# Kernel tuning notes

Hardware: AMD Instinct MI355X
Metric: run time of the kernel (lower is better)

The kernel has to match this reference:

```python
import jax, jax.numpy as jnp
import numpy as np

STRIDE = (1, 2, 2)
PADDING = ((2, 2), (3, 3), (3, 3))


def setup_inputs() -> dict:
    key = jax.random.key(0)
    kx, kw, kb = jax.random.split(key, 3)
    x = jax.random.normal(kx, (8, 3, 16, 112, 112), dtype=jnp.float32)
    weight = jax.random.normal(kw, (64, 3, 5, 7, 7), dtype=jnp.float32)
    bias = jax.random.normal(kb, (64,), dtype=jnp.float32)
    return {"x": x, "weight": weight, "bias": bias}


def reference(x, weight, bias):
    # NCDHW input, OIDHW weight -> NCDHW output; same math as the
    # torch module's explicit slice-multiply-sum conv3d.
    out = jax.lax.conv_general_dilated(
        x, weight,
        window_strides=STRIDE,
        padding=PADDING,
        dimension_numbers=("NCDHW", "OIDHW", "NCDHW"),
    )
    out = out + bias[None, :, None, None, None]
    return out
```

## Files before the change

### kernel.cpp

```cpp
#include <hip/hip_runtime.h>


typedef __attribute__((ext_vector_type(8)))  short short8;
typedef __attribute__((ext_vector_type(4)))  float f32x4;
typedef __attribute__((ext_vector_type(16))) float f32x16;

#define CI 3
#define DI 16
#define HI 112
#define WI 112
#define CO 64
#define DO_ 16
#define HO 56
#define WO 56
#define HW_IN 12544
#define DHWO 50176

#define NROW 105
#define NCH 27

#define XP_ROW 120
#define XP_H   119
#define XP_D   20
#define XPAD_BYTES  (8*3*XP_D*XP_H*XP_ROW*2)
#define WBUF_OFF    XPAD_BYTES
#define WS_NEED     (WBUF_OFF + NCH*4*64*16 + 4096)

#define SEG_SH 1080
#define SEG_DW 540
#define ROW_DW 60

__device__ __forceinline__ unsigned short f2bf(float f) {
    unsigned u = __float_as_uint(f);
    return (unsigned short)((u + 0x7FFFu + ((u >> 16) & 1u)) >> 16);
}
__device__ __forceinline__ unsigned pk_bf16(float a, float b) {
    unsigned r;
    asm("v_cvt_pk_bf16_f32 %0, %1, %2" : "=v"(r) : "v"(a), "v"(b));
    return r;
}

__device__ __forceinline__ constexpr int rb2(int r) {
    const int rc = (r > 104) ? 104 : r;
    const int c  = rc / 35;
    const int kd = (rc / 7) % 5;
    const int kh = rc % 7;
    return (c * 6 + kd) * SEG_DW + kh * ROW_DW;
}

#define XP_THREADS (8*3*XP_D*XP_H*15)
#define XP_BLOCKS  3347

__global__ void prep_all(const float* __restrict__ x, const float* __restrict__ wgt,
                         unsigned* __restrict__ xp, short8* __restrict__ wbuf) {
    if (blockIdx.x < XP_BLOCKS) {
        const int g = blockIdx.x * 256 + threadIdx.x;
        if (g >= XP_THREADS) return;
        const int s8 = g % 15;
        int r = g / 15;
        const int hp = r % XP_H; r /= XP_H;
        const int dp = r % XP_D; r /= XP_D;
        const int c  = r % 3;
        const int n  = r / 3;
        const int din = dp - 2, hin = hp - 3;
        const bool rowok = ((unsigned)din < (unsigned)DI) && ((unsigned)hin < (unsigned)HI);
        float v[8];
        const int w0 = 8 * s8 - 3;
        if (rowok && s8 >= 1 && s8 <= 13) {
            const float* xr = x + ((n * CI + c) * DI + din) * HW_IN + hin * WI + w0;
            #pragma unroll
            for (int j = 0; j < 8; ++j) v[j] = xr[j];
        } else if (rowok && (s8 == 0 || s8 == 14)) {
            const float* xr = x + ((n * CI + c) * DI + din) * HW_IN + hin * WI;
            #pragma unroll
            for (int j = 0; j < 8; ++j) {
                const int w = w0 + j;
                v[j] = ((unsigned)w < (unsigned)WI) ? xr[w] : 0.0f;
            }
        } else {
            #pragma unroll
            for (int j = 0; j < 8; ++j) v[j] = 0.0f;
        }
        uint4 o;
        o.x = pk_bf16(v[0], v[1]); o.y = pk_bf16(v[2], v[3]);
        o.z = pk_bf16(v[4], v[5]); o.w = pk_bf16(v[6], v[7]);
        *reinterpret_cast<uint4*>(xp + 4 * (size_t)g) = o;
    } else {
        const int t = (blockIdx.x - XP_BLOCKS) * 256 + threadIdx.x;
        const int lane = t & 63;
        const int cf   = t >> 6;
        const int q    = cf & 3;
        const int a    = q & 1;
        const int ks   = q >> 1;
        const int ch   = cf >> 2;
        const int l31  = lane & 31;
        const int hl   = lane >> 5;
        const int co   = a * 32 + l31;
        const int r    = ch * 4 + ks * 2 + hl;
        const int rc   = (r > 104) ? 104 : r;
        const int c    = rc / 35;
        const int kd   = (rc / 7) % 5;
        const int kh   = rc % 7;
        const float* wsrc = wgt + (((co * CI + c) * 5 + kd) * 7 + kh) * 7;
        short8 v;
        #pragma unroll
        for (int j = 0; j < 8; ++j) {
            float w = (r < NROW && j < 7) ? wsrc[j] : 0.0f;
            v[j] = (short)f2bf(w);
        }
        wbuf[(size_t)cf * 64 + lane] = v;
    }
}

#define MFMA32(A, B, C) __builtin_amdgcn_mfma_f32_32x32x16_bf16(A, B, C, 0, 0, 0)

__launch_bounds__(256, 4)
__global__ void conv3d_v13(const unsigned short* __restrict__ xpad,
                           const short8* __restrict__ wbuf,
                           const float* __restrict__ bias,
                           float* __restrict__ out) {
    __shared__ __align__(16) unsigned short xl[18 * SEG_SH + 128];

    const int tid = threadIdx.x;
    int b = ((blockIdx.x & 7) * 224) + (blockIdx.x >> 3);
    const int ht  = b % 28;  b /= 28;
    const int ddp = b & 7;
    const int n   = b >> 3;
    const int ho0 = ht * 2;
    const int dd0 = ddp * 2;

    const int lane = tid & 63;
    const int wid  = tid >> 6;

    {
        const size_t nb = (size_t)(n * CI) * XP_D;
        for (int s = wid; s < 18; s += 4) {
            const int c = s / 6;
            const int p = s - c * 6;
            const char* gsrc = (const char*)(xpad +
                ((nb + (size_t)c * XP_D + (dd0 + p)) * XP_H + 2 * ho0) * XP_ROW)
                + lane * 16;
            char* ldst = (char*)&xl[s * SEG_SH];
            __builtin_amdgcn_global_load_lds(
                (const __attribute__((address_space(1))) void*)(gsrc),
                (__attribute__((address_space(3))) void*)(ldst), 16, 0, 0);
            __builtin_amdgcn_global_load_lds(
                (const __attribute__((address_space(1))) void*)(gsrc + 1024),
                (__attribute__((address_space(3))) void*)(ldst + 1024), 16, 0, 0);
            if (lane < 7)
                __builtin_amdgcn_global_load_lds(
                    (const __attribute__((address_space(1))) void*)(gsrc + 2048),
                    (__attribute__((address_space(3))) void*)(ldst + 2048), 16, 0, 0);
        }
    }

    const int ddl = wid & 1;
    const int hoL = wid >> 1;
    const int l31 = lane & 31;
    const int hl  = lane >> 5;
    const int tspB = ddl * SEG_DW + hoL * (2 * ROW_DW) + l31;

    f32x16 acc[2][2];
    #pragma unroll
    for (int a = 0; a < 2; ++a) {
        f32x16 bv;
        #pragma unroll
        for (int g = 0; g < 16; ++g)
            bv[g] = bias[a * 32 + (g & 3) + 8 * (g >> 2) + 4 * hl];
        acc[a][0] = bv; acc[a][1] = bv;
    }

    const short8* wbp = wbuf + lane;
    const unsigned* xlu = reinterpret_cast<const unsigned*>(xl);

    union BxU { unsigned u[4]; short8 s; };
    short8 As[2][4];
    BxU    Bs[4];

    auto loadA = [&](int ch, int slot) {
        const int nq = (ch == NCH - 1) ? 2 : 4;
        #pragma unroll
        for (int q = 0; q < 4; ++q)
            if (q < nq) As[slot][q] = wbp[(ch * 4 + q) * 64];
    };
    auto loadB = [&](int ch) {
        const int nks = (ch == NCH - 1) ? 1 : 2;
        #pragma unroll
        for (int ks = 0; ks < 2; ++ks) {
            if (ks < nks) {
                const int r0 = ch * 4 + ks * 2;
                const int b0 = rb2(r0);
                const int b1 = rb2(r0 + 1);
                const int base = b0 + hl * (b1 - b0);
                const unsigned* xp = xlu + base + tspB;
                #pragma unroll
                for (int f = 0; f < 2; ++f) {
                    const unsigned* p = xp + f * 32;
                    Bs[ks * 2 + f].u[0] = p[0];
                    Bs[ks * 2 + f].u[1] = p[1];
                    Bs[ks * 2 + f].u[2] = p[2];
                    Bs[ks * 2 + f].u[3] = p[3];
                }
            }
        }
    };

    loadA(0, 0);
    __syncthreads();

    #pragma unroll
    for (int ch = 0; ch < NCH; ++ch) {
        loadB(ch);
        if (ch + 1 < NCH) loadA(ch + 1, (ch + 1) & 1);
        __builtin_amdgcn_s_setprio(1);
        const int s = ch & 1;
        #pragma unroll
        for (int a = 0; a < 2; ++a) {
            #pragma unroll
            for (int f = 0; f < 2; ++f) {
                acc[a][f] = MFMA32(As[s][0 + a], Bs[0 + f].s, acc[a][f]);
                if (ch != NCH - 1)
                    acc[a][f] = MFMA32(As[s][2 + a], Bs[2 + f].s, acc[a][f]);
            }
        }
        __builtin_amdgcn_s_setprio(0);
    }

    const int dd = dd0 + ddl;
    const int ho = ho0 + hoL;
    const size_t obase = (size_t)n * CO * DHWO + (size_t)dd * 3136 + ho * WO;
    #pragma unroll
    for (int f = 0; f < 2; ++f) {
        const int wo = f * 32 + l31;
        if (f == 0 || l31 < 24) {
            #pragma unroll
            for (int a = 0; a < 2; ++a) {
                #pragma unroll
                for (int g = 0; g < 16; ++g) {
                    const int co = a * 32 + (g & 3) + 8 * (g >> 2) + 4 * hl;
                    out[obase + (size_t)co * DHWO + wo] = acc[a][f][g];
                }
            }
        }
    }
}

#define FB_LR 13
#define FB_LROWS 234
#define FB_LWS 144
#define FB_XLSZ (FB_LROWS*FB_LWS)
#define MFMA16(A, B, C) __builtin_amdgcn_mfma_f32_16x16x32_bf16(A, B, C, 0, 0, 0)

__global__ void prep_weights_fb(const float* __restrict__ wgt, short8* __restrict__ wbuf) {
    const int t    = blockIdx.x * 64 + threadIdx.x;
    const int lane = t & 63;
    const int cf   = t >> 6;
    const int l15  = lane & 15;
    const int kgrp = lane >> 4;
    const int co   = (cf & 3) * 16 + l15;
    const int rr   = (cf >> 2) * 4 + kgrp;
    const int rc   = (rr < NROW) ? rr : (NROW - 1);
    const int c    = rc / 35;
    const int kd   = (rc / 7) % 5;
    const int kh   = rc % 7;
    const float* wsrc = wgt + (((co * CI + c) * 5 + kd) * 7 + kh) * 7;
    short8 v;
    #pragma unroll
    for (int j = 0; j < 8; ++j) {
        float w = (rr < NROW && j < 7) ? wsrc[j] : 0.0f;
        v[j] = (short)f2bf(w);
    }
    wbuf[(size_t)cf * 64 + lane] = v;
}

__launch_bounds__(512, 2)
__global__ void conv3d_mfma4(const float* __restrict__ x,
                             const short8* __restrict__ wbuf,
                             const float* __restrict__ bias,
                             float* __restrict__ out) {
    __shared__ unsigned short xl[FB_XLSZ];
    __shared__ int rowg[FB_LROWS];
    __shared__ unsigned short tabr[108];

    const int tid = threadIdx.x;
    int b = blockIdx.x;
    const int ht  = b % 14;  b /= 14;
    const int ddp = b % 8;
    const int n   = b / 8;
    const int ho0 = ht * 4;
    const int dd0 = ddp * 2;

    if (tid < FB_LROWS) {
        const int c   = tid / (6 * FB_LR);
        const int rem = tid - c * (6 * FB_LR);
        const int p   = rem / FB_LR;
        const int rl  = rem - p * FB_LR;
        const int din = dd0 - 2 + p;
        const int hin = 2 * ho0 - 3 + rl;
        const bool ok = ((unsigned)din < (unsigned)DI) && ((unsigned)hin < (unsigned)HI);
        rowg[tid] = ok ? ((n * CI + c) * DI + din) * HW_IN + hin * WI : -1;
    }
    if (tid < 108) {
        const int rc = (tid < NROW) ? tid : (NROW - 1);
        const int c  = rc / 35;
        const int kd = (rc / 7) % 5;
        const int kh = rc % 7;
        tabr[tid] = (unsigned short)(((c * 6 + kd) * FB_LR + kh) * FB_LWS);
    }
    __syncthreads();

    const int lane = tid & 63;
    const int wid  = tid >> 6;

    for (int row = wid; row < FB_LROWS; row += 8) {
        const int base = rowg[row];
        unsigned short* dst = &xl[row * FB_LWS];
        if (lane < 57) {
            float v0 = 0.0f, v1 = 0.0f;
            const int w0 = 2 * lane - 1;
            if (base >= 0) {
                if (lane >= 1)  v0 = x[base + w0];
                if (lane <= 55) v1 = x[base + w0 + 1];
            }
            *reinterpret_cast<unsigned*>(&dst[2 * lane + 2]) = pk_bf16(v0, v1);
        } else {
            const int dw = (lane == 57) ? 0 : lane;
            *reinterpret_cast<unsigned*>(&dst[2 * dw]) = 0u;
        }
    }
    __syncthreads();

    const int ddl  = wid & 1;
    const int hoL  = wid >> 1;
    const int l15  = lane & 15;
    const int kgrp = lane >> 4;
    const int woff = ddl * (FB_LR * FB_LWS) + hoL * (2 * FB_LWS);

    f32x4 acc[4][4];
    #pragma unroll
    for (int a = 0; a < 4; ++a) {
        f32x4 bv;
        #pragma unroll
        for (int r = 0; r < 4; ++r) bv[r] = bias[a * 16 + kgrp * 4 + r];
        #pragma unroll
        for (int f = 0; f < 4; ++f) acc[a][f] = bv;
    }

    const short8* wbp = wbuf + lane;
    short8 Acur[4], Anxt[4];
    #pragma unroll
    for (int a = 0; a < 4; ++a) Acur[a] = wbp[a * 64];
    int tb = (int)tabr[kgrp] + woff;

    const unsigned* xlu = reinterpret_cast<const unsigned*>(xl);

    for (int ch = 0; ch < NCH; ++ch) {
        int tbn = 0;
        if (ch + 1 < NCH) {
            tbn = (int)tabr[(ch + 1) * 4 + kgrp] + woff;
            #pragma unroll
            for (int a = 0; a < 4; ++a) Anxt[a] = wbp[((ch + 1) * 4 + a) * 64];
        }
        const unsigned* xp = xlu + (tb >> 1) + l15;
        union { unsigned u[4]; short8 s; } bx[4];
        #pragma unroll
        for (int f = 0; f < 4; ++f) {
            const unsigned* p = xp + f * 16;
            bx[f].u[0] = p[0]; bx[f].u[1] = p[1];
            bx[f].u[2] = p[2]; bx[f].u[3] = p[3];
        }
        #pragma unroll
        for (int f = 0; f < 4; ++f) {
            acc[0][f] = MFMA16(Acur[0], bx[f].s, acc[0][f]);
            acc[1][f] = MFMA16(Acur[1], bx[f].s, acc[1][f]);
            acc[2][f] = MFMA16(Acur[2], bx[f].s, acc[2][f]);
            acc[3][f] = MFMA16(Acur[3], bx[f].s, acc[3][f]);
        }
        tb = tbn;
        #pragma unroll
        for (int a = 0; a < 4; ++a) Acur[a] = Anxt[a];
    }

    const int dd = dd0 + ddl;
    const int ho = ho0 + hoL;
    #pragma unroll
    for (int f = 0; f < 4; ++f) {
        const int wo = f * 16 + l15;
        if (f < 3 || l15 < 8) {
            float* op = out + (((size_t)(n * CO) * DO_ + dd) * HO + ho) * WO + wo;
            #pragma unroll
            for (int a = 0; a < 4; ++a) {
                const int co = a * 16 + kgrp * 4;
                #pragma unroll
                for (int r = 0; r < 4; ++r)
                    op[(size_t)(co + r) * DHWO] = acc[a][f][r];
            }
        }
    }
}

extern "C" void kernel_launch(void* const* d_in, const int* in_sizes, int n_in,
                              void* d_out, int out_size, void* d_ws, size_t ws_size,
                              hipStream_t stream) {
    const float* x    = (const float*)d_in[0];
    const float* wgt  = (const float*)d_in[1];
    const float* bias = (const float*)d_in[2];
    float* out        = (float*)d_out;

    if (ws_size >= (size_t)WS_NEED) {
        unsigned* xpad = (unsigned*)d_ws;
        short8* wbuf   = (short8*)((char*)d_ws + WBUF_OFF);
        hipLaunchKernelGGL(prep_all, dim3(XP_BLOCKS + 27, 1, 1), dim3(256, 1, 1), 0,
                           stream, x, wgt, xpad, wbuf);
        hipLaunchKernelGGL(conv3d_v13, dim3(1792, 1, 1), dim3(256, 1, 1), 0, stream,
                           (const unsigned short*)xpad, wbuf, bias, out);
    } else {
        short8* wbuf = (short8*)d_ws;
        hipLaunchKernelGGL(prep_weights_fb, dim3(NCH * 4, 1, 1), dim3(64, 1, 1), 0,
                           stream, wgt, wbuf);
        hipLaunchKernelGGL(conv3d_mfma4, dim3(896, 1, 1), dim3(512, 1, 1), 0, stream,
                           x, wbuf, bias, out);
    }
}
```

Measured before the change: 67.69 us.

## Load conv input tiles directly from global memory, dropping LDS staging

The conv kernel no longer stages the padded input slab into shared memory with global_load_lds and a barrier. Each lane now reads its B fragments straight from the padded bf16 buffer in global memory as 16-byte vector loads. A three-slot register ring prefetches B two chunks ahead to hide the global latency. This removes the LDS fill and the __syncthreads, but it relies on L1/L2 for the heavy input reuse across overlapping windows and raises register pressure, so the launch bounds drop from 4 to 3 blocks per CU.

```diff
diff --git a/kernel.cpp b/kernel.cpp
--- a/kernel.cpp
+++ b/kernel.cpp
@@ -26,9 +26,10 @@
 #define WBUF_OFF    XPAD_BYTES
 #define WS_NEED     (WBUF_OFF + NCH*4*64*16 + 4096)
 
-#define SEG_SH 1080
-#define SEG_DW 540
 #define ROW_DW 60
+#define DP_DW  (XP_H*ROW_DW)
+#define C_DW   (XP_D*DP_DW)
+#define N_DW   (CI*C_DW)
 
 __device__ __forceinline__ unsigned short f2bf(float f) {
     unsigned u = __float_as_uint(f);
@@ -40,12 +41,12 @@
     return r;
 }
 
-__device__ __forceinline__ constexpr int rb2(int r) {
+__device__ __forceinline__ constexpr int G(int r) {
     const int rc = (r > 104) ? 104 : r;
     const int c  = rc / 35;
     const int kd = (rc / 7) % 5;
     const int kh = rc % 7;
-    return (c * 6 + kd) * SEG_DW + kh * ROW_DW;
+    return c * C_DW + kd * DP_DW + kh * ROW_DW;
 }
 
 #define XP_THREADS (8*3*XP_D*XP_H*15)
@@ -114,13 +115,11 @@
 
 #define MFMA32(A, B, C) __builtin_amdgcn_mfma_f32_32x32x16_bf16(A, B, C, 0, 0, 0)
 
-__launch_bounds__(256, 4)
-__global__ void conv3d_v13(const unsigned short* __restrict__ xpad,
+__launch_bounds__(256, 3)
+__global__ void conv3d_v16(const unsigned* __restrict__ xdw,
                            const short8* __restrict__ wbuf,
                            const float* __restrict__ bias,
                            float* __restrict__ out) {
-    __shared__ __align__(16) unsigned short xl[18 * SEG_SH + 128];
-
     const int tid = threadIdx.x;
     int b = ((blockIdx.x & 7) * 224) + (blockIdx.x >> 3);
     const int ht  = b % 28;  b /= 28;
@@ -132,33 +131,13 @@
     const int lane = tid & 63;
     const int wid  = tid >> 6;
 
-    {
-        const size_t nb = (size_t)(n * CI) * XP_D;
-        for (int s = wid; s < 18; s += 4) {
-            const int c = s / 6;
-            const int p = s - c * 6;
-            const char* gsrc = (const char*)(xpad +
-                ((nb + (size_t)c * XP_D + (dd0 + p)) * XP_H + 2 * ho0) * XP_ROW)
-                + lane * 16;
-            char* ldst = (char*)&xl[s * SEG_SH];
-            __builtin_amdgcn_global_load_lds(
-                (const __attribute__((address_space(1))) void*)(gsrc),
-                (__attribute__((address_space(3))) void*)(ldst), 16, 0, 0);
-            __builtin_amdgcn_global_load_lds(
-                (const __attribute__((address_space(1))) void*)(gsrc + 1024),
-                (__attribute__((address_space(3))) void*)(ldst + 1024), 16, 0, 0);
-            if (lane < 7)
-                __builtin_amdgcn_global_load_lds(
-                    (const __attribute__((address_space(1))) void*)(gsrc + 2048),
-                    (__attribute__((address_space(3))) void*)(ldst + 2048), 16, 0, 0);
-        }
-    }
-
     const int ddl = wid & 1;
     const int hoL = wid >> 1;
     const int l31 = lane & 31;
     const int hl  = lane >> 5;
-    const int tspB = ddl * SEG_DW + hoL * (2 * ROW_DW) + l31;
+    const int dd  = dd0 + ddl;
+    const int ho  = ho0 + hoL;
+    const int wbase = n * N_DW + dd * DP_DW + ho * (2 * ROW_DW) + l31;
 
     f32x16 acc[2][2];
     #pragma unroll
@@ -171,11 +150,11 @@
     }
 
     const short8* wbp = wbuf + lane;
-    const unsigned* xlu = reinterpret_cast<const unsigned*>(xl);
+    const unsigned* xw = xdw + wbase;
 
     union BxU { unsigned u[4]; short8 s; };
     short8 As[2][4];
-    BxU    Bs[4];
+    BxU    Bs[3][4];
 
     auto loadA = [&](int ch, int slot) {
         const int nq = (ch == NCH - 1) ? 2 : 4;
@@ -183,51 +162,50 @@
         for (int q = 0; q < 4; ++q)
             if (q < nq) As[slot][q] = wbp[(ch * 4 + q) * 64];
     };
-    auto loadB = [&](int ch) {
+    auto loadB = [&](int ch, int slot) {
         const int nks = (ch == NCH - 1) ? 1 : 2;
         #pragma unroll
         for (int ks = 0; ks < 2; ++ks) {
             if (ks < nks) {
                 const int r0 = ch * 4 + ks * 2;
-                const int b0 = rb2(r0);
-                const int b1 = rb2(r0 + 1);
-                const int base = b0 + hl * (b1 - b0);
-                const unsigned* xp = xlu + base + tspB;
+                const int g0 = G(r0);
+                const int g1 = G(r0 + 1);
+                const unsigned* p0 = xw + (g0 + hl * (g1 - g0));
                 #pragma unroll
                 for (int f = 0; f < 2; ++f) {
-                    const unsigned* p = xp + f * 32;
-                    Bs[ks * 2 + f].u[0] = p[0];
-                    Bs[ks * 2 + f].u[1] = p[1];
-                    Bs[ks * 2 + f].u[2] = p[2];
-                    Bs[ks * 2 + f].u[3] = p[3];
+                    uint4 v = *reinterpret_cast<const uint4*>(p0 + f * 32);
+                    Bs[slot][ks * 2 + f].u[0] = v.x;
+                    Bs[slot][ks * 2 + f].u[1] = v.y;
+                    Bs[slot][ks * 2 + f].u[2] = v.z;
+                    Bs[slot][ks * 2 + f].u[3] = v.w;
                 }
             }
         }
     };
 
     loadA(0, 0);
-    __syncthreads();
+    loadB(0, 0);
+    loadB(1, 1);
 
     #pragma unroll
     for (int ch = 0; ch < NCH; ++ch) {
-        loadB(ch);
+        if (ch + 2 < NCH) loadB(ch + 2, (ch + 2) % 3);
         if (ch + 1 < NCH) loadA(ch + 1, (ch + 1) & 1);
         __builtin_amdgcn_s_setprio(1);
-        const int s = ch & 1;
+        const int sA = ch & 1;
+        const int sB = ch % 3;
         #pragma unroll
         for (int a = 0; a < 2; ++a) {
             #pragma unroll
             for (int f = 0; f < 2; ++f) {
-                acc[a][f] = MFMA32(As[s][0 + a], Bs[0 + f].s, acc[a][f]);
+                acc[a][f] = MFMA32(As[sA][0 + a], Bs[sB][0 + f].s, acc[a][f]);
                 if (ch != NCH - 1)
-                    acc[a][f] = MFMA32(As[s][2 + a], Bs[2 + f].s, acc[a][f]);
+                    acc[a][f] = MFMA32(As[sA][2 + a], Bs[sB][2 + f].s, acc[a][f]);
             }
         }
         __builtin_amdgcn_s_setprio(0);
     }
 
-    const int dd = dd0 + ddl;
-    const int ho = ho0 + hoL;
     const size_t obase = (size_t)n * CO * DHWO + (size_t)dd * 3136 + ho * WO;
     #pragma unroll
     for (int f = 0; f < 2; ++f) {
@@ -412,8 +390,8 @@
         short8* wbuf   = (short8*)((char*)d_ws + WBUF_OFF);
         hipLaunchKernelGGL(prep_all, dim3(XP_BLOCKS + 27, 1, 1), dim3(256, 1, 1), 0,
                            stream, x, wgt, xpad, wbuf);
-        hipLaunchKernelGGL(conv3d_v13, dim3(1792, 1, 1), dim3(256, 1, 1), 0, stream,
-                           (const unsigned short*)xpad, wbuf, bias, out);
+        hipLaunchKernelGGL(conv3d_v16, dim3(1792, 1, 1), dim3(256, 1, 1), 0, stream,
+                           xpad, wbuf, bias, out);
     } else {
         short8* wbuf = (short8*)d_ws;
         hipLaunchKernelGGL(prep_weights_fb, dim3(NCH * 4, 1, 1), dim3(64, 1, 1), 0,
```

Measured after the change: 77.92 us. 1.15x slower.

## Double block to 512 threads, 4 output rows, stage weights in LDS

Applied to the files above, without the earlier changes.

Each block now covers four output rows instead of two using 8 waves, so the staged input halo (13 rows vs 9) is shared over more output rows. This cuts redundant global-to-LDS input traffic. Weight fragments move from per-wave global loads to a double-buffered LDS stage filled by global_load_lds, one wave per chunk. That adds a __syncthreads per chunk, which may stall the MFMA pipeline and lower overlap.

```diff
diff --git a/kernel.cpp b/kernel.cpp
--- a/kernel.cpp
+++ b/kernel.cpp
@@ -26,9 +26,11 @@
 #define WBUF_OFF    XPAD_BYTES
 #define WS_NEED     (WBUF_OFF + NCH*4*64*16 + 4096)
 
-#define SEG_SH 1080
-#define SEG_DW 540
-#define ROW_DW 60
+#define LR 13
+#define SEG_SH (LR*XP_ROW)
+#define SEG_DW (SEG_SH/2)
+#define ROW_DW (XP_ROW/2)
+#define ALDS_SH (18*SEG_SH + 128)
 
 __device__ __forceinline__ unsigned short f2bf(float f) {
     unsigned u = __float_as_uint(f);
@@ -113,20 +115,23 @@
 }
 
 #define MFMA32(A, B, C) __builtin_amdgcn_mfma_f32_32x32x16_bf16(A, B, C, 0, 0, 0)
-
-__launch_bounds__(256, 4)
-__global__ void conv3d_v13(const unsigned short* __restrict__ xpad,
+#define GLDS(src, dst) __builtin_amdgcn_global_load_lds( \
+    (const __attribute__((address_space(1))) void*)(src), \
+    (__attribute__((address_space(3))) void*)(dst), 16, 0, 0)
+
+__launch_bounds__(512, 4)
+__global__ void conv3d_v17(const unsigned short* __restrict__ xpad,
                            const short8* __restrict__ wbuf,
                            const float* __restrict__ bias,
                            float* __restrict__ out) {
-    __shared__ __align__(16) unsigned short xl[18 * SEG_SH + 128];
+    __shared__ __align__(16) unsigned short xl[ALDS_SH + 4096];
 
     const int tid = threadIdx.x;
-    int b = ((blockIdx.x & 7) * 224) + (blockIdx.x >> 3);
-    const int ht  = b % 28;  b /= 28;
+    int b = ((blockIdx.x & 7) * 112) + (blockIdx.x >> 3);
+    const int ht  = b % 14;  b /= 14;
     const int ddp = b & 7;
     const int n   = b >> 3;
-    const int ho0 = ht * 2;
+    const int ho0 = ht * 4;
     const int dd0 = ddp * 2;
 
     const int lane = tid & 63;
@@ -134,31 +139,32 @@
 
     {
         const size_t nb = (size_t)(n * CI) * XP_D;
-        for (int s = wid; s < 18; s += 4) {
+        for (int s = wid; s < 18; s += 8) {
             const int c = s / 6;
             const int p = s - c * 6;
             const char* gsrc = (const char*)(xpad +
                 ((nb + (size_t)c * XP_D + (dd0 + p)) * XP_H + 2 * ho0) * XP_ROW)
                 + lane * 16;
             char* ldst = (char*)&xl[s * SEG_SH];
-            __builtin_amdgcn_global_load_lds(
-                (const __attribute__((address_space(1))) void*)(gsrc),
-                (__attribute__((address_space(3))) void*)(ldst), 16, 0, 0);
-            __builtin_amdgcn_global_load_lds(
-                (const __attribute__((address_space(1))) void*)(gsrc + 1024),
-                (__attribute__((address_space(3))) void*)(ldst + 1024), 16, 0, 0);
-            if (lane < 7)
-                __builtin_amdgcn_global_load_lds(
-                    (const __attribute__((address_space(1))) void*)(gsrc + 2048),
-                    (__attribute__((address_space(3))) void*)(ldst + 2048), 16, 0, 0);
-        }
-    }
+            GLDS(gsrc, ldst);
+            GLDS(gsrc + 1024, ldst + 1024);
+            GLDS(gsrc + 2048, ldst + 2048);
+            if (lane < 3) GLDS(gsrc + 3072, ldst + 3072);
+        }
+    }
+    if (wid == 0) {
+        const char* gs = (const char*)wbuf + lane * 16;
+        char* ad = (char*)&xl[ALDS_SH];
+        GLDS(gs, ad); GLDS(gs + 1024, ad + 1024);
+        GLDS(gs + 2048, ad + 2048); GLDS(gs + 3072, ad + 3072);
+    }
+    __syncthreads();
 
     const int ddl = wid & 1;
-    const int hoL = wid >> 1;
+    const int hp  = wid >> 1;
     const int l31 = lane & 31;
     const int hl  = lane >> 5;
-    const int tspB = ddl * SEG_DW + hoL * (2 * ROW_DW) + l31;
+    const int tspB = ddl * SEG_DW + hp * (2 * ROW_DW) + l31;
 
     f32x16 acc[2][2];
     #pragma unroll
@@ -170,64 +176,57 @@
         acc[a][0] = bv; acc[a][1] = bv;
     }
 
-    const short8* wbp = wbuf + lane;
     const unsigned* xlu = reinterpret_cast<const unsigned*>(xl);
-
     union BxU { unsigned u[4]; short8 s; };
-    short8 As[2][4];
-    BxU    Bs[4];
-
-    auto loadA = [&](int ch, int slot) {
-        const int nq = (ch == NCH - 1) ? 2 : 4;
-        #pragma unroll
-        for (int q = 0; q < 4; ++q)
-            if (q < nq) As[slot][q] = wbp[(ch * 4 + q) * 64];
-    };
-    auto loadB = [&](int ch) {
-        const int nks = (ch == NCH - 1) ? 1 : 2;
+
+    #pragma unroll
+    for (int ch = 0; ch < NCH; ++ch) {
+        if (ch + 1 < NCH && wid == ((ch + 1) & 7)) {
+            const char* gs = (const char*)(wbuf + (size_t)(ch + 1) * 4 * 64) + lane * 16;
+            char* ad = (char*)&xl[ALDS_SH] + ((ch + 1) & 1) * 4096;
+            GLDS(gs, ad); GLDS(gs + 1024, ad + 1024);
+            GLDS(gs + 2048, ad + 2048); GLDS(gs + 3072, ad + 3072);
+        }
+        short8 As[4];
+        {
+            const char* ab = (const char*)&xl[ALDS_SH] + (ch & 1) * 4096 + lane * 16;
+            As[0] = *reinterpret_cast<const short8*>(ab);
+            As[1] = *reinterpret_cast<const short8*>(ab + 1024);
+            As[2] = *reinterpret_cast<const short8*>(ab + 2048);
+            As[3] = *reinterpret_cast<const short8*>(ab + 3072);
+        }
+        BxU Bs[4];
         #pragma unroll
         for (int ks = 0; ks < 2; ++ks) {
-            if (ks < nks) {
-                const int r0 = ch * 4 + ks * 2;
-                const int b0 = rb2(r0);
-                const int b1 = rb2(r0 + 1);
-                const int base = b0 + hl * (b1 - b0);
-                const unsigned* xp = xlu + base + tspB;
-                #pragma unroll
-                for (int f = 0; f < 2; ++f) {
-                    const unsigned* p = xp + f * 32;
-                    Bs[ks * 2 + f].u[0] = p[0];
-                    Bs[ks * 2 + f].u[1] = p[1];
-                    Bs[ks * 2 + f].u[2] = p[2];
-                    Bs[ks * 2 + f].u[3] = p[3];
-                }
-            }
-        }
-    };
-
-    loadA(0, 0);
-    __syncthreads();
-
-    #pragma unroll
-    for (int ch = 0; ch < NCH; ++ch) {
-        loadB(ch);
-        if (ch + 1 < NCH) loadA(ch + 1, (ch + 1) & 1);
+            const int r0 = ch * 4 + ks * 2;
+            const int b0 = rb2(r0);
+            const int b1 = rb2(r0 + 1);
+            const int base = b0 + hl * (b1 - b0);
+            const unsigned* xp = xlu + base + tspB;
+            #pragma unroll
+            for (int f = 0; f < 2; ++f) {
+                const unsigned* p = xp + f * 32;
+                Bs[ks * 2 + f].u[0] = p[0];
+                Bs[ks * 2 + f].u[1] = p[1];
+                Bs[ks * 2 + f].u[2] = p[2];
+                Bs[ks * 2 + f].u[3] = p[3];
+            }
+        }
         __builtin_amdgcn_s_setprio(1);
-        const int s = ch & 1;
         #pragma unroll
         for (int a = 0; a < 2; ++a) {
             #pragma unroll
             for (int f = 0; f < 2; ++f) {
-                acc[a][f] = MFMA32(As[s][0 + a], Bs[0 + f].s, acc[a][f]);
-                if (ch != NCH - 1)
-                    acc[a][f] = MFMA32(As[s][2 + a], Bs[2 + f].s, acc[a][f]);
+                acc[a][f] = MFMA32(As[0 + a], Bs[0 + f].s, acc[a][f]);
+                acc[a][f] = MFMA32(As[2 + a], Bs[2 + f].s, acc[a][f]);
             }
         }
         __builtin_amdgcn_s_setprio(0);
+        if (ch != NCH - 1) __syncthreads();
     }
 
     const int dd = dd0 + ddl;
-    const int ho = ho0 + hoL;
+    const int ho = ho0 + hp;
     const size_t obase = (size_t)n * CO * DHWO + (size_t)dd * 3136 + ho * WO;
     #pragma unroll
     for (int f = 0; f < 2; ++f) {
@@ -412,7 +411,7 @@
         short8* wbuf   = (short8*)((char*)d_ws + WBUF_OFF);
         hipLaunchKernelGGL(prep_all, dim3(XP_BLOCKS + 27, 1, 1), dim3(256, 1, 1), 0,
                            stream, x, wgt, xpad, wbuf);
-        hipLaunchKernelGGL(conv3d_v13, dim3(1792, 1, 1), dim3(256, 1, 1), 0, stream,
+        hipLaunchKernelGGL(conv3d_v17, dim3(896, 1, 1), dim3(512, 1, 1), 0, stream,
                            (const unsigned short*)xpad, wbuf, bias, out);
     } else {
         short8* wbuf = (short8*)d_ws;
```

Measured after the change: 64.94 us. 4.1% less time.
